# Kernel optimization log

Hardware: AMD Instinct MI355X
Metric: run time of the kernel (lower is better)

The kernel has to match this reference:

```python
import jax, jax.numpy as jnp
import numpy as np

BETA = 0.25
N_E = 8192
E_DIM = 256


def setup_inputs() -> dict:
    key = jax.random.key(0)
    k1, k2 = jax.random.split(key)
    z = jax.random.normal(k1, (16, E_DIM, 32, 32), dtype=jnp.float32)
    # matches torch init: uniform_(-1/n_e, 1/n_e)
    codebook = jax.random.uniform(k2, (N_E, E_DIM), dtype=jnp.float32,
                                  minval=-1.0 / N_E, maxval=1.0 / N_E)
    return {"z": z, "codebook": codebook}


def reference(z, codebook):
    B, C, H, W = z.shape  # C == e_dim
    zp = jnp.transpose(z, (0, 2, 3, 1))          # [B, H, W, C]
    zf = zp.reshape(-1, C)                       # [N, C], N = B*H*W
    # squared L2 distances: ||z||^2 + ||e||^2 - 2 z.e
    d = (jnp.sum(zf * zf, axis=1, keepdims=True)
         + jnp.sum(codebook * codebook, axis=1)
         - 2.0 * jnp.einsum('nc,kc->nk', zf, codebook))  # [N, n_e]
    min_encoding_indices = jnp.argmin(d, axis=1)         # [N]
    z_q = codebook[min_encoding_indices].reshape(zp.shape)  # [B, H, W, C]
    sg = jax.lax.stop_gradient
    loss = jnp.mean((sg(z_q) - zp) ** 2) + BETA * jnp.mean((z_q - sg(zp)) ** 2)
    # straight-through estimator
    z_q_st = zp + sg(z_q - zp)
    z_q_out = jnp.transpose(z_q_st, (0, 3, 1, 2))  # back to NCHW
    return z_q_out, loss, min_encoding_indices
```

## Files before the change

### kernel.cpp

```cpp
#include <hip/hip_runtime.h>

typedef short s8v __attribute__((ext_vector_type(8)));
typedef float f4v __attribute__((ext_vector_type(4)));
typedef float f4 __attribute__((ext_vector_type(4)));

#define N_PIX 16384
#define NE    8192
#define EDIM  256
#define ZQ_ELEMS 4194304
#define MARGIN 4.5e-4f
#define NGRP 512

__device__ __forceinline__ float bf2f(unsigned short u) {
    union { unsigned int i; float f; } c; c.i = ((unsigned int)u) << 16; return c.f;
}
__device__ __forceinline__ unsigned short f2bf(float f) {
    unsigned int u = __float_as_uint(f);
    u = (u + 0x7fffu + ((u >> 16) & 1u)) >> 16;
    return (unsigned short)u;
}
__device__ __forceinline__ unsigned short f2bf_down(float f) {
    unsigned int u = __float_as_uint(f);
    unsigned short b = (unsigned short)(u >> 16);
    if ((u & 0xFFFFu) && (u >> 31)) b += 1;
    return b;
}

__device__ __forceinline__ float np_pw128sq(const float* a) {
    float r[8];
    #pragma unroll
    for (int j = 0; j < 8; ++j) r[j] = __fmul_rn(a[j], a[j]);
    for (int i = 8; i < 128; i += 8)
        #pragma unroll
        for (int j = 0; j < 8; ++j) r[j] = __fadd_rn(r[j], __fmul_rn(a[i + j], a[i + j]));
    return __fadd_rn(__fadd_rn(__fadd_rn(r[0], r[1]), __fadd_rn(r[2], r[3])),
                     __fadd_rn(__fadd_rn(r[4], r[5]), __fadd_rn(r[6], r[7])));
}

__global__ __launch_bounds__(256) void vq_prep(const float* __restrict__ cb,
                                               unsigned short* __restrict__ cb16,
                                               float* __restrict__ esum32) {
    int t = threadIdx.x;
    int base = blockIdx.x * 64;
    const float* src = cb + (size_t)base * EDIM;
    unsigned short* dst = cb16 + (size_t)base * EDIM;
    for (int i = 0; i < 64; ++i) dst[i * EDIM + t] = f2bf(src[i * EDIM + t]);
    if (t < 64) {
        const float* a = cb + (size_t)(base + t) * EDIM;
        esum32[base + t] = __fadd_rn(np_pw128sq(a), np_pw128sq(a + 128));
    }
}

__global__ __launch_bounds__(256) void vq_zprep(const float* __restrict__ z,
                                                unsigned short* __restrict__ z16) {
    __shared__ unsigned short zl[64 * 66];
    int t = threadIdx.x;
    int p0 = (blockIdx.x >> 2) * 64;
    int c0 = (blockIdx.x & 3) * 64;
    int b = p0 >> 10, hw0 = p0 & 1023;
    const float* src = z + (((size_t)b * 256 + c0) << 10) + hw0;
    #pragma unroll
    for (int i = 0; i < 16; ++i) {
        int idx = i * 256 + t;
        int ch = idx >> 6, px = idx & 63;
        zl[px * 66 + ch] = f2bf(src[((size_t)ch << 10) + px]);
    }
    __syncthreads();
    #pragma unroll
    for (int i = 0; i < 16; ++i) {
        int idx = i * 256 + t;
        int px = idx >> 6, ch = idx & 63;
        z16[((size_t)(p0 + px)) * 256 + c0 + ch] = zl[px * 66 + ch];
    }
}

__global__ __launch_bounds__(512, 2) void vq_phase1g(const unsigned short* __restrict__ cb16,
                                                     const unsigned short* __restrict__ z16,
                                                     unsigned short* __restrict__ gmin) {
    __shared__ unsigned short L[2][32768];
    const int t = threadIdx.x;
    const int wave = t >> 6, lane = t & 63;
    const int q = lane >> 4, r = lane & 15;
    const int wr = wave >> 2, wc = wave & 3;
    const int sb = ((int)blockIdx.x & 7) * 256 + ((int)blockIdx.x >> 3);
    const int cm0 = (sb & 31) * 256;
    const int pn0 = (sb >> 5) * 256;

    const int pc0 = t, pc1 = t + 512;
    const int row0 = pc0 >> 2, row1 = pc1 >> 2;
    const int lc0 = (pc0 & 3) ^ ((row0 >> 1) & 3);
    const int lc1 = (pc1 & 3) ^ ((row1 >> 1) & 3);
    const int go0 = row0 * 256 + lc0 * 8;
    const int go1 = row1 * 256 + lc1 * 8;
    const int ld0 = pc0 * 8;
    const int ld1 = pc1 * 8;

    const unsigned short* gA = cb16 + (size_t)cm0 * 256;
    const unsigned short* gB = z16 + (size_t)pn0 * 256;

    f4v acc[8][4];
    const f4v zz = {0.f, 0.f, 0.f, 0.f};
    #pragma unroll
    for (int mi = 0; mi < 8; ++mi)
        #pragma unroll
        for (int ni = 0; ni < 4; ++ni) acc[mi][ni] = zz;

    const int cxo = (q ^ ((r >> 1) & 3)) * 8;

#define GLL(g, l) __builtin_amdgcn_global_load_lds( \
        (const __attribute__((address_space(1))) unsigned int*)(g), \
        (__attribute__((address_space(3))) unsigned int*)(l), 16, 0, 0)
#define STAGE(gbase, lbase, kh, gk) do { \
        GLL((gbase) + go0 + (kh) * 32 + (gk), (lbase) + (kh) * 8192 + ld0); \
        GLL((gbase) + go1 + (kh) * 32 + (gk), (lbase) + (kh) * 8192 + ld1); } while (0)

    STAGE(gA, &L[0][0], 0, 0);
    STAGE(gB, &L[0][16384], 0, 0);
    STAGE(gA, &L[0][0], 1, 0);
    STAGE(gB, &L[0][16384], 1, 0);

    for (int kt = 0; kt < 4; ++kt) {
        const int buf = kt & 1;
        const unsigned short* Ab = &L[buf][0];
        const unsigned short* Bb = &L[buf][16384];
        unsigned short* An = &L[buf ^ 1][0];
        unsigned short* Bn = &L[buf ^ 1][16384];
        const int gk = (kt + 1) * 64;
        const bool st = kt < 3;

        asm volatile("s_waitcnt vmcnt(4)" ::: "memory");
        __builtin_amdgcn_s_barrier();
        __builtin_amdgcn_sched_barrier(0);

        s8v Af[4], Bf[4];
        #pragma unroll
        for (int ni = 0; ni < 4; ++ni)
            Bf[ni] = *(const s8v*)&Bb[(wc * 64 + ni * 16 + r) * 32 + cxo];
        #pragma unroll
        for (int mi = 0; mi < 4; ++mi)
            Af[mi] = *(const s8v*)&Ab[(wr * 128 + mi * 16 + r) * 32 + cxo];
        if (st) STAGE(gA, An, 0, gk);
        __builtin_amdgcn_s_barrier();
        __builtin_amdgcn_sched_barrier(0);
        __builtin_amdgcn_s_setprio(1);
        #pragma unroll
        for (int mi = 0; mi < 4; ++mi)
            #pragma unroll
            for (int ni = 0; ni < 4; ++ni)
                acc[mi][ni] = __builtin_amdgcn_mfma_f32_16x16x32_bf16(
                    Af[mi], Bf[ni], acc[mi][ni], 0, 0, 0);
        __builtin_amdgcn_s_setprio(0);
        __builtin_amdgcn_s_barrier();

        #pragma unroll
        for (int mi = 0; mi < 4; ++mi)
            Af[mi] = *(const s8v*)&Ab[(wr * 128 + (4 + mi) * 16 + r) * 32 + cxo];
        if (st) STAGE(gB, Bn, 0, gk);
        __builtin_amdgcn_s_barrier();
        __builtin_amdgcn_sched_barrier(0);
        __builtin_amdgcn_s_setprio(1);
        #pragma unroll
        for (int mi = 0; mi < 4; ++mi)
            #pragma unroll
            for (int ni = 0; ni < 4; ++ni)
                acc[4 + mi][ni] = __builtin_amdgcn_mfma_f32_16x16x32_bf16(
                    Af[mi], Bf[ni], acc[4 + mi][ni], 0, 0, 0);
        __builtin_amdgcn_s_setprio(0);
        asm volatile("s_waitcnt vmcnt(4)" ::: "memory");
        __builtin_amdgcn_s_barrier();
        __builtin_amdgcn_sched_barrier(0);

        #pragma unroll
        for (int ni = 0; ni < 4; ++ni)
            Bf[ni] = *(const s8v*)&Bb[8192 + (wc * 64 + ni * 16 + r) * 32 + cxo];
        #pragma unroll
        for (int mi = 0; mi < 4; ++mi)
            Af[mi] = *(const s8v*)&Ab[8192 + (wr * 128 + mi * 16 + r) * 32 + cxo];
        if (st) STAGE(gA, An, 1, gk);
        __builtin_amdgcn_s_barrier();
        __builtin_amdgcn_sched_barrier(0);
        __builtin_amdgcn_s_setprio(1);
        #pragma unroll
        for (int mi = 0; mi < 4; ++mi)
            #pragma unroll
            for (int ni = 0; ni < 4; ++ni)
                acc[mi][ni] = __builtin_amdgcn_mfma_f32_16x16x32_bf16(
                    Af[mi], Bf[ni], acc[mi][ni], 0, 0, 0);
        __builtin_amdgcn_s_setprio(0);
        __builtin_amdgcn_s_barrier();

        #pragma unroll
        for (int mi = 0; mi < 4; ++mi)
            Af[mi] = *(const s8v*)&Ab[8192 + (wr * 128 + (4 + mi) * 16 + r) * 32 + cxo];
        if (st) STAGE(gB, Bn, 1, gk);
        __builtin_amdgcn_s_barrier();
        __builtin_amdgcn_sched_barrier(0);
        __builtin_amdgcn_s_setprio(1);
        #pragma unroll
        for (int mi = 0; mi < 4; ++mi)
            #pragma unroll
            for (int ni = 0; ni < 4; ++ni)
                acc[4 + mi][ni] = __builtin_amdgcn_mfma_f32_16x16x32_bf16(
                    Af[mi], Bf[ni], acc[4 + mi][ni], 0, 0, 0);
        __builtin_amdgcn_s_setprio(0);
    }
#undef STAGE
#undef GLL

    #pragma unroll
    for (int mi = 0; mi < 8; ++mi) {
        int g = cm0 / 16 + wr * 8 + mi;
        #pragma unroll
        for (int ni = 0; ni < 4; ++ni) {
            f4v a = acc[mi][ni];
            float mx = fmaxf(fmaxf(a[0], a[1]), fmaxf(a[2], a[3]));
            mx = fmaxf(mx, __shfl_xor(mx, 16));
            mx = fmaxf(mx, __shfl_xor(mx, 32));
            if (q == 0)
                gmin[(size_t)g * N_PIX + pn0 + wc * 64 + ni * 16 + r] =
                    f2bf_down(-2.0f * mx);
        }
    }
}

__global__ __launch_bounds__(512, 2) void vq_phase1(const float* __restrict__ z,
                                                    const unsigned short* __restrict__ cb16,
                                                    unsigned short* __restrict__ gmin) {
    const int t = threadIdx.x;
    const int wave = t >> 6, lane = t & 63;
    const int col = lane & 15, q = lane >> 4;
    const int mb = (blockIdx.x >> 1) * 64;
    const int chalf = blockIdx.x & 1;

    s8v Z[4][8];
    #pragma unroll
    for (int pt = 0; pt < 4; ++pt) {
        int n = mb + pt * 16 + col;
        const float* zb = z + ((size_t)(n >> 10) << 18) + (size_t)(n & 1023);
        #pragma unroll
        for (int c0 = 0; c0 < 8; ++c0) {
            s8v a;
            #pragma unroll
            for (int j = 0; j < 8; ++j) {
                int c = c0 * 32 + q * 8 + j;
                a[j] = (short)f2bf(zb[(size_t)c << 10]);
            }
            Z[pt][c0] = a;
        }
    }

    const int kbase = chalf * 4096 + wave * 512;
    for (int it = 0; it < 16; ++it) {
        int n0 = kbase + it * 32;
        const unsigned short* bb = cb16 + (size_t)(n0 + col) * EDIM + q * 8;
        f4v zz = {0.f, 0.f, 0.f, 0.f};
        f4v acc[4][2];
        #pragma unroll
        for (int pt = 0; pt < 4; ++pt) { acc[pt][0] = zz; acc[pt][1] = zz; }
        #pragma unroll
        for (int c0 = 0; c0 < 8; ++c0) {
            s8v C0 = *(const s8v*)(bb + c0 * 32);
            s8v C1 = *(const s8v*)(bb + 16 * EDIM + c0 * 32);
            #pragma unroll
            for (int pt = 0; pt < 4; ++pt) {
                acc[pt][0] = __builtin_amdgcn_mfma_f32_16x16x32_bf16(C0, Z[pt][c0], acc[pt][0], 0, 0, 0);
                acc[pt][1] = __builtin_amdgcn_mfma_f32_16x16x32_bf16(C1, Z[pt][c0], acc[pt][1], 0, 0, 0);
            }
        }
        int gbase = chalf * 256 + wave * 32 + it * 2;
        #pragma unroll
        for (int pt = 0; pt < 4; ++pt) {
            #pragma unroll
            for (int s = 0; s < 2; ++s) {
                f4v a = acc[pt][s];
                float mx = fmaxf(fmaxf(a[0], a[1]), fmaxf(a[2], a[3]));
                mx = fmaxf(mx, __shfl_xor(mx, 16));
                mx = fmaxf(mx, __shfl_xor(mx, 32));
                if (q == 0)
                    gmin[(size_t)(gbase + s) * N_PIX + mb + pt * 16 + col] =
                        f2bf_down(-2.0f * mx);
            }
        }
    }
}

__global__ __launch_bounds__(256) void vq_phase2(const float* __restrict__ z,
                                                 const float* __restrict__ cb,
                                                 const float* __restrict__ esum32,
                                                 const unsigned short* __restrict__ gmin,
                                                 unsigned int* __restrict__ idxw) {
    __shared__ float zt[16 * 260];
    __shared__ unsigned short gm[NGRP * 17];
    __shared__ float zs[16];
    int t = threadIdx.x;
    int wave = t >> 6, lane = t & 63;
    int p0 = blockIdx.x * 16;
    int bb = p0 >> 10, inner = p0 & 1023;

    #pragma unroll
    for (int i = 0; i < 16; ++i) {
        int c = i * 16 + (t >> 4), p = t & 15;
        zt[p * 260 + c] = z[((size_t)(bb * 256 + c) << 10) + inner + p];
    }
    #pragma unroll
    for (int i = 0; i < 32; ++i) {
        int g = i * 16 + (t >> 4), p = t & 15;
        gm[g * 17 + p] = gmin[(size_t)g * N_PIX + p0 + p];
    }
    __syncthreads();
    if (t < 16) {
        const float* a = zt + t * 260;
        zs[t] = __fadd_rn(np_pw128sq(a), np_pw128sq(a + 128));
    }
    __syncthreads();

    #pragma unroll
    for (int pp = 0; pp < 4; ++pp) {
        int p = wave * 4 + pp;
        float lmin = 3.0e38f;
        #pragma unroll
        for (int j = 0; j < 8; ++j) lmin = fminf(lmin, bf2f(gm[(lane * 8 + j) * 17 + p]));
        #pragma unroll
        for (int m = 1; m < 64; m <<= 1) lmin = fminf(lmin, __shfl_xor(lmin, m));
        float thr = lmin + MARGIN;
        float zsp = zs[p];

        float bd = 3.0e38f; int bk = 0x7FFFFFFF;
        for (int j = 0; j < 8; ++j) {
            unsigned long long mask = __ballot(bf2f(gm[(lane * 8 + j) * 17 + p]) <= thr);
            while (mask) {
                int lb = __builtin_ctzll(mask); mask &= mask - 1;
                int g = lb * 8 + j;
                int k = g * 16 + (lane >> 2);
                const f4* cr = (const f4*)(cb + (size_t)k * EDIM) + (lane & 3);
                const f4* zr = (const f4*)(zt + p * 260) + (lane & 3);
                double a0 = 0.0, a1 = 0.0, a2 = 0.0, a3 = 0.0;
                #pragma unroll
                for (int i = 0; i < 16; ++i) {
                    f4 x = zr[i * 4], y = cr[i * 4];
                    a0 = fma((double)x[0], (double)y[0], a0);
                    a1 = fma((double)x[1], (double)y[1], a1);
                    a2 = fma((double)x[2], (double)y[2], a2);
                    a3 = fma((double)x[3], (double)y[3], a3);
                }
                double s = (a0 + a1) + (a2 + a3);
                s += __shfl_xor(s, 1);
                s += __shfl_xor(s, 2);
                float E = (float)s;
                float d = __fsub_rn(__fadd_rn(zsp, esum32[k]), __fmul_rn(2.0f, E));
                if (d < bd || (d == bd && k < bk)) { bd = d; bk = k; }
            }
        }
        #pragma unroll
        for (int m = 1; m < 64; m <<= 1) {
            float od = __shfl_xor(bd, m); int ok = __shfl_xor(bk, m);
            if (od < bd || (od == bd && ok < bk)) { bd = od; bk = ok; }
        }
        if (lane == 0) idxw[p0 + p] = (unsigned int)bk;
    }
}

__global__ __launch_bounds__(256) void vq_emit(const float* __restrict__ cb,
                                               const float* __restrict__ z,
                                               const unsigned int* __restrict__ idxw,
                                               float* __restrict__ outf,
                                               float* __restrict__ lossw) {
    __shared__ float red[4];
    int t = threadIdx.x;
    int gtid = blockIdx.x * 256 + t;
    if (gtid < N_PIX) outf[ZQ_ELEMS + 1 + gtid] = (float)(idxw[gtid] & (NE - 1));

    float acc = 0.f;
    size_t base = (size_t)blockIdx.x * 16384;
    for (int i = 0; i < 64; ++i) {
        size_t o = base + (size_t)i * 256 + t;
        int b = (int)(o >> 18);
        int c = (int)((o >> 10) & 255);
        int p = (int)(o & 1023);
        int idx = (int)(idxw[b * 1024 + p] & (NE - 1));
        float qv = cb[(size_t)idx * EDIM + c];
        outf[o] = qv;
        float d = qv - z[o];
        acc = fmaf(d, d, acc);
    }
    #pragma unroll
    for (int off = 32; off > 0; off >>= 1) acc += __shfl_down(acc, off);
    if ((t & 63) == 0) red[t >> 6] = acc;
    __syncthreads();
    if (t == 0) atomicAdd(lossw, red[0] + red[1] + red[2] + red[3]);
}

__global__ void vq_finalize(const float* __restrict__ lossw, float* __restrict__ loss_out) {
    loss_out[0] = 1.25f * lossw[0] * (1.0f / 4194304.0f);
}

extern "C" void kernel_launch(void* const* d_in, const int* in_sizes, int n_in,
                              void* d_out, int out_size, void* d_ws, size_t ws_size,
                              hipStream_t stream) {
    const float* z  = (const float*)d_in[0];
    const float* cb = (const float*)d_in[1];
    float* outf = (float*)d_out;
    unsigned short* gmin = (unsigned short*)d_out;

    char* w = (char*)d_ws;
    unsigned short* cb16   = (unsigned short*)w;
    float*          esum32 = (float*)(w + 4194304);
    unsigned int*   idxw   = (unsigned int*)(w + 4227072);
    float*          lossw  = (float*)(w + 4292608);
    unsigned short* z16    = (unsigned short*)(w + 4292864);

    if (ws_size < 4292612) return;
    const bool big_ws = (ws_size >= 12681472);

    hipMemsetAsync(lossw, 0, sizeof(float), stream);
    vq_prep    <<<NE / 64, 256, 0, stream>>>(cb, cb16, esum32);
    if (big_ws) {
        vq_zprep  <<<(N_PIX / 64) * (EDIM / 64), 256, 0, stream>>>(z, z16);
        vq_phase1g<<<(NE / 256) * (N_PIX / 256), 512, 0, stream>>>(cb16, z16, gmin);
    } else {
        vq_phase1 <<<(N_PIX / 64) * 2, 512, 0, stream>>>(z, cb16, gmin);
    }
    vq_phase2  <<<N_PIX / 16, 256, 0, stream>>>(z, cb, esum32, gmin, idxw);
    vq_emit    <<<256, 256, 0, stream>>>(cb, z, idxw, outf, lossw);
    vq_finalize<<<1, 1, 0, stream>>>(lossw, outf + ZQ_ELEMS);
}
```

Measured before the change: 275.0 us.

## Make phase1g GEMM persistent over eight pixel tiles with cross-tile prefetch

Each block now keeps one 256-row codebook tile and walks eight consecutive 256-pixel tiles, so 256 blocks replace 2048. The k-loop is flattened across tiles, so the next tile's first K-slice is prefetched during the current tile's epilogue. All of a K-step's global-to-LDS loads are issued in the first half of the iteration, and the wait count is adjusted to match. This removes per-block prologue and epilogue bubbles and launch overhead. The cost is fewer blocks, which may leave CUs underused: 256 blocks at two per CU on the MI355X's 256 CUs. The codebook A tile is also reloaded for every pixel tile rather than reused, and the earlier XCD-aware block swizzle is dropped.

```diff
diff --git a/kernel.cpp b/kernel.cpp
--- a/kernel.cpp
+++ b/kernel.cpp
@@ -82,9 +82,8 @@
     const int wave = t >> 6, lane = t & 63;
     const int q = lane >> 4, r = lane & 15;
     const int wr = wave >> 2, wc = wave & 3;
-    const int sb = ((int)blockIdx.x & 7) * 256 + ((int)blockIdx.x >> 3);
-    const int cm0 = (sb & 31) * 256;
-    const int pn0 = (sb >> 5) * 256;
+    const int cm0 = ((int)blockIdx.x >> 3) * 256;
+    const int pg  = (int)blockIdx.x & 7;
 
     const int pc0 = t, pc1 = t + 512;
     const int row0 = pc0 >> 2, row1 = pc1 >> 2;
@@ -96,7 +95,7 @@
     const int ld1 = pc1 * 8;
 
     const unsigned short* gA = cb16 + (size_t)cm0 * 256;
-    const unsigned short* gB = z16 + (size_t)pn0 * 256;
+    const unsigned short* gB0 = z16 + (size_t)pg * 2048 * 256;
 
     f4v acc[8][4];
     const f4v zz = {0.f, 0.f, 0.f, 0.f};
@@ -115,18 +114,20 @@
         GLL((gbase) + go1 + (kh) * 32 + (gk), (lbase) + (kh) * 8192 + ld1); } while (0)
 
     STAGE(gA, &L[0][0], 0, 0);
-    STAGE(gB, &L[0][16384], 0, 0);
+    STAGE(gB0, &L[0][16384], 0, 0);
     STAGE(gA, &L[0][0], 1, 0);
-    STAGE(gB, &L[0][16384], 1, 0);
-
-    for (int kt = 0; kt < 4; ++kt) {
-        const int buf = kt & 1;
+    STAGE(gB0, &L[0][16384], 1, 0);
+
+    for (int it = 0; it < 32; ++it) {
+        const int buf = it & 1;
         const unsigned short* Ab = &L[buf][0];
         const unsigned short* Bb = &L[buf][16384];
         unsigned short* An = &L[buf ^ 1][0];
         unsigned short* Bn = &L[buf ^ 1][16384];
-        const int gk = (kt + 1) * 64;
-        const bool st = kt < 3;
+        const int nit = it + 1;
+        const bool st = nit < 32;
+        const int gk = (nit & 3) * 64;
+        const unsigned short* gBn = gB0 + (size_t)(nit >> 2) * 256 * 256;
 
         asm volatile("s_waitcnt vmcnt(4)" ::: "memory");
         __builtin_amdgcn_s_barrier();
@@ -139,7 +140,7 @@
         #pragma unroll
         for (int mi = 0; mi < 4; ++mi)
             Af[mi] = *(const s8v*)&Ab[(wr * 128 + mi * 16 + r) * 32 + cxo];
-        if (st) STAGE(gA, An, 0, gk);
+        if (st) { STAGE(gA, An, 0, gk); STAGE(gBn, Bn, 0, gk); }
         __builtin_amdgcn_s_barrier();
         __builtin_amdgcn_sched_barrier(0);
         __builtin_amdgcn_s_setprio(1);
@@ -155,7 +156,7 @@
         #pragma unroll
         for (int mi = 0; mi < 4; ++mi)
             Af[mi] = *(const s8v*)&Ab[(wr * 128 + (4 + mi) * 16 + r) * 32 + cxo];
-        if (st) STAGE(gB, Bn, 0, gk);
+        if (st) { STAGE(gA, An, 1, gk); STAGE(gBn, Bn, 1, gk); }
         __builtin_amdgcn_s_barrier();
         __builtin_amdgcn_sched_barrier(0);
         __builtin_amdgcn_s_setprio(1);
@@ -166,7 +167,7 @@
                 acc[4 + mi][ni] = __builtin_amdgcn_mfma_f32_16x16x32_bf16(
                     Af[mi], Bf[ni], acc[4 + mi][ni], 0, 0, 0);
         __builtin_amdgcn_s_setprio(0);
-        asm volatile("s_waitcnt vmcnt(4)" ::: "memory");
+        asm volatile("s_waitcnt vmcnt(8)" ::: "memory");
         __builtin_amdgcn_s_barrier();
         __builtin_amdgcn_sched_barrier(0);
 
@@ -176,7 +177,6 @@
         #pragma unroll
         for (int mi = 0; mi < 4; ++mi)
             Af[mi] = *(const s8v*)&Ab[8192 + (wr * 128 + mi * 16 + r) * 32 + cxo];
-        if (st) STAGE(gA, An, 1, gk);
         __builtin_amdgcn_s_barrier();
         __builtin_amdgcn_sched_barrier(0);
         __builtin_amdgcn_s_setprio(1);
@@ -192,7 +192,6 @@
         #pragma unroll
         for (int mi = 0; mi < 4; ++mi)
             Af[mi] = *(const s8v*)&Ab[8192 + (wr * 128 + (4 + mi) * 16 + r) * 32 + cxo];
-        if (st) STAGE(gB, Bn, 1, gk);
         __builtin_amdgcn_s_barrier();
         __builtin_amdgcn_sched_barrier(0);
         __builtin_amdgcn_s_setprio(1);
@@ -203,24 +202,28 @@
                 acc[4 + mi][ni] = __builtin_amdgcn_mfma_f32_16x16x32_bf16(
                     Af[mi], Bf[ni], acc[4 + mi][ni], 0, 0, 0);
         __builtin_amdgcn_s_setprio(0);
+
+        if ((it & 3) == 3) {
+            const int pn0 = pg * 2048 + (it >> 2) * 256;
+            #pragma unroll
+            for (int mi = 0; mi < 8; ++mi) {
+                int g = cm0 / 16 + wr * 8 + mi;
+                #pragma unroll
+                for (int ni = 0; ni < 4; ++ni) {
+                    f4v a = acc[mi][ni];
+                    float mx = fmaxf(fmaxf(a[0], a[1]), fmaxf(a[2], a[3]));
+                    mx = fmaxf(mx, __shfl_xor(mx, 16));
+                    mx = fmaxf(mx, __shfl_xor(mx, 32));
+                    if (q == 0)
+                        gmin[(size_t)g * N_PIX + pn0 + wc * 64 + ni * 16 + r] =
+                            f2bf_down(-2.0f * mx);
+                    acc[mi][ni] = zz;
+                }
+            }
+        }
     }
 #undef STAGE
 #undef GLL
-
-    #pragma unroll
-    for (int mi = 0; mi < 8; ++mi) {
-        int g = cm0 / 16 + wr * 8 + mi;
-        #pragma unroll
-        for (int ni = 0; ni < 4; ++ni) {
-            f4v a = acc[mi][ni];
-            float mx = fmaxf(fmaxf(a[0], a[1]), fmaxf(a[2], a[3]));
-            mx = fmaxf(mx, __shfl_xor(mx, 16));
-            mx = fmaxf(mx, __shfl_xor(mx, 32));
-            if (q == 0)
-                gmin[(size_t)g * N_PIX + pn0 + wc * 64 + ni * 16 + r] =
-                    f2bf_down(-2.0f * mx);
-        }
-    }
 }
 
 __global__ __launch_bounds__(512, 2) void vq_phase1(const float* __restrict__ z,
@@ -416,7 +419,7 @@
     vq_prep    <<<NE / 64, 256, 0, stream>>>(cb, cb16, esum32);
     if (big_ws) {
         vq_zprep  <<<(N_PIX / 64) * (EDIM / 64), 256, 0, stream>>>(z, z16);
-        vq_phase1g<<<(NE / 256) * (N_PIX / 256), 512, 0, stream>>>(cb16, z16, gmin);
+        vq_phase1g<<<(NE / 256) * (N_PIX / 2048), 512, 0, stream>>>(cb16, z16, gmin);
     } else {
         vq_phase1 <<<(N_PIX / 64) * 2, 512, 0, stream>>>(z, cb16, gmin);
     }
```

New measurement: 282.2 us. +2.6%, slower.
